# Kernel tuning notes

Hardware: AMD Instinct MI355X
Metric: run time of the kernel (lower is better)

Reference implementation:

```python
import jax, jax.numpy as jnp
import numpy as np

B = 4096
NUM_PTS = 1000

def de_boor(knotss, t, CP, p):
    # knotss: [N, K], t: [T, N], CP: [N, ncp, 2, 1] -> [T, N, 2, 1]
    N = knotss.shape[0]
    # k[b] = number of knots in knotss[b, p+1:] strictly below t (matches torch loop)
    k = jnp.sum((t[:, :, None] > knotss[None, :, p + 1:]).astype(jnp.int32), axis=-1)  # [T, N]
    bn = jnp.arange(N)[None, :, None]
    idx = k[:, :, None] + jnp.arange(p + 1)[None, None, :]           # [T, N, p+1]
    E = CP[bn, idx]                                                  # [T, N, p+1, 2, 1]
    te = t[:, :, None, None, None]
    for j in range(1, p + 1):
        m = p - j + 1
        i = jnp.arange(m)[None, None, :]
        a1 = knotss[bn, p + 1 + i + k[:, :, None]][..., None, None]  # [T, N, m, 1, 1]
        a2 = knotss[bn, i + j + k[:, :, None]][..., None, None]
        # in torch, ascending i reads old E[i+1]; vectorized update over old E is identical
        E = ((a1 - te) * E[:, :, :m] + (te - a2) * E[:, :, 1:m + 1]) / (a1 - a2)
    return E[:, :, 0]

def first_derivative(Pc, knots):
    n = Pc.shape[1]
    den = (knots[:, 4:n + 3] - knots[:, 1:n])[:, :, None, None]
    Q = 3.0 / den * (Pc[:, 1:] - Pc[:, :-1])
    return Q, knots[:, 1:-1]

def second_derivative(Q, knots):
    n = Q.shape[1]
    den = (knots[:, 3:n + 2] - knots[:, 1:n])[:, :, None, None]
    R = 2.0 / den * (Q[:, 1:] - Q[:, :-1])
    return R, knots[:, 1:-1]

def construct(t, knots, p=3):
    # t: [B], knots: [B, K] -> N: [B, K-1]; replicates stale-tail behavior of torch loop
    K = knots.shape[1]
    N = ((t[:, None] >= knots[:, :-1]) & (t[:, None] < knots[:, 1:])).astype(knots.dtype)
    lenN = K - 2
    for power in range(1, p + 1):
        m = lenN - power
        den_a = knots[:, power:power + m] - knots[:, :m]
        a = jnp.where(den_a != 0, (t[:, None] - knots[:, :m]) / jnp.where(den_a != 0, den_a, 1.0), 0.0)
        den_b = knots[:, power + 1:power + 1 + m] - knots[:, 1:1 + m]
        b = jnp.where(den_b != 0, (knots[:, power + 1:power + 1 + m] - t[:, None]) / jnp.where(den_b != 0, den_b, 1.0), 0.0)
        N = N.at[:, :m].set(N[:, :m] * a + N[:, 1:m + 1] * b)
    return N

def construct_A(knots):
    # knots: [B, 12], 6 data points -> A: [B, 8, 8]
    Bn = knots.shape[0]
    rows = [construct(knots[:, i + 3], knots) for i in range(5)]
    # i == 5 hits the knots[0, 8] == 1 branch (clamped right end): one-hot at column 7
    row5 = jnp.zeros((Bn, knots.shape[1] - 1), knots.dtype).at[:, 7].set(1.0)
    A = jnp.stack(rows + [row5], axis=1)[:, :, :8]                   # [B, 6, 8]
    z = jnp.zeros((Bn, 1, 8), knots.dtype)
    A = jnp.concatenate([z, A, z], axis=1)                           # [B, 8, 8]
    A = A.at[:, 0, 0].add(knots[:, 5]).at[:, 0, 1].add(-knots[:, 4] - knots[:, 5]).at[:, 0, 2].add(knots[:, 4])
    A = A.at[:, -1, -3].add(1.0 - knots[:, 7]).at[:, -1, -2].add(knots[:, 7] + knots[:, 6] - 2.0).at[:, -1, -1].add(1.0 - knots[:, 6])
    return A

def solve(P, knots):
    Bn = P.shape[0]
    z = jnp.zeros((Bn, 1, 1), P.dtype)
    Px = jnp.concatenate([z, P[:, :, 0], z], axis=1)  # [B, 8, 1]
    Py = jnp.concatenate([z, P[:, :, 1], z], axis=1)
    inv = jnp.linalg.inv(construct_A(knots))
    Cx = inv @ Px
    Cy = inv @ Py
    return jnp.concatenate([Cx, Cy], axis=2)[..., None]  # [B, 8, 2, 1]

def forward(x, P, W1, b1, W2, b2, W3, b3):
    h = jax.nn.relu(x @ W1.T + b1)
    h = jax.nn.relu(h @ W2.T + b2)
    xs = jax.nn.softmax(h @ W3.T + b3, axis=1)  # [B, 5]
    # torch: w[:, i] = x[:, i] + detach(w[:, i-1]) -> cumsum in value, identity in grad
    x4 = xs[:, :4]
    w = x4 + jax.lax.stop_gradient(jnp.cumsum(x4, axis=1) - x4)
    Bn = x.shape[0]
    knots = jnp.concatenate([jnp.zeros((Bn, 4), x.dtype), w, jnp.ones((Bn, 4), x.dtype)], axis=1)  # [B, 12]
    C = solve(P, knots)  # [B, 8, 2, 1]
    # global curvature over linspace(knots[0,3]=0, knots[0,10]=1, NUM_PTS)
    L = jnp.linspace(0.0, 1.0, NUM_PTS).astype(x.dtype)
    tall = jnp.broadcast_to(L[:, None], (NUM_PTS, Bn))
    Q, dk = first_derivative(C, knots)
    R, ddk = second_derivative(Q, dk)
    sp = de_boor(dk, tall, Q, 2)    # [T, B, 2, 1] spline'
    sdp = de_boor(ddk, tall, R, 1)  # [T, B, 2, 1] spline''
    spx, spy = sp[:, :, 0, 0], sp[:, :, 1, 0]
    sdx, sdy = sdp[:, :, 0, 0], sdp[:, :, 1, 0]
    speed2 = spx ** 2 + spy ** 2
    curv = (spx * sdy - spy * sdx) / (speed2 ** 3) ** 0.5
    vals = curv ** 2 * jnp.sqrt(speed2)  # [T, B]; de_boor(knots2, J, Q, 2) == spline', reused
    S1 = vals[1::2].sum(axis=0)
    S2 = vals[0::2].sum(axis=0)
    h_step = 1.0 / (NUM_PTS - 1)
    integration = h_step / 3.0 * (4.0 * S1 + 2.0 * S2)
    return integration, knots

def setup_inputs():
    key = jax.random.key(0)
    ks = jax.random.split(key, 8)
    return {
        "x": jax.random.normal(ks[0], (B, 8), jnp.float32),
        "P": jax.random.normal(ks[1], (B, 6, 2, 1), jnp.float32),
        "W1": jax.random.normal(ks[2], (128, 8), jnp.float32) * 0.3,
        "b1": jnp.full((128,), 0.01, jnp.float32),
        "W2": jax.random.normal(ks[3], (128, 128), jnp.float32) * 0.09,
        "b2": jnp.full((128,), 0.01, jnp.float32),
        "W3": jax.random.normal(ks[4], (5, 128), jnp.float32) * 0.1,
        "b3": jnp.full((5,), 0.01, jnp.float32),
    }

def reference(x, P, W1, b1, W2, b2, W3, b3):
    return forward(x, P, W1, b1, W2, b2, W3, b3)
```

## Files before the change

### kernel.cpp

```cpp
#include <hip/hip_runtime.h>
#include <math.h>

#define BATCH 4096
#define NPTS 1000

#define WSYNC() do { asm volatile("s_waitcnt lgkmcnt(0)" ::: "memory"); \
                     __builtin_amdgcn_sched_barrier(0); } while (0)

__device__ __forceinline__ float frcp(float v) { return __builtin_amdgcn_rcpf(v); }

__global__ __launch_bounds__(256, 2) void net2_one(
    const float* __restrict__ x, const float* __restrict__ P,
    const float* __restrict__ W1, const float* __restrict__ b1,
    const float* __restrict__ W2, const float* __restrict__ b2,
    const float* __restrict__ W3, const float* __restrict__ b3,
    float* __restrict__ out_integ, float* __restrict__ out_knots)
{
    __shared__ float4 s_w2[4096];
    __shared__ float s_h1[8][128];
    __shared__ float s_part[4][4][5];
    __shared__ float LA[8][8][10];
    __shared__ float LQ[8][16];
    __shared__ float LR[8][16];
    __shared__ float s_coef[8][64];

    const int tid = threadIdx.x;
    const int wv = tid >> 6, lane = tid & 63;
    const int p = tid >> 7, row = tid & 127;
    const int b0 = blockIdx.x * 8;

    {
        const float4* W2v = (const float4*)W2;
        #pragma unroll
        for (int it = 0; it < 16; ++it) {
            int f = it * 256 + tid;
            int j = f >> 5, c4 = f & 31;
            s_w2[j * 32 + (c4 ^ (j & 7))] = W2v[f];
        }
    }

    {
        float4 w0 = ((const float4*)(W1 + row * 8))[0];
        float4 w1 = ((const float4*)(W1 + row * 8))[1];
        float bb = b1[row];
        #pragma unroll
        for (int k = 0; k < 4; ++k) {
            const float* xr = x + (b0 + p * 4 + k) * 8;
            float4 xa = ((const float4*)xr)[0];
            float4 xb = ((const float4*)xr)[1];
            float h = bb + w0.x*xa.x + w0.y*xa.y + w0.z*xa.z + w0.w*xa.w
                         + w1.x*xb.x + w1.y*xb.y + w1.z*xb.z + w1.w*xb.w;
            s_h1[p * 4 + k][row] = fmaxf(h, 0.f);
        }
    }
    __syncthreads();

    float bb2 = b2[row];
    float a0 = bb2, a1 = bb2, a2 = bb2, a3 = bb2;
    {
        const float4* wrow = s_w2 + row * 32;
        const int rx = row & 7;
        const float4* h0 = (const float4*)s_h1[p * 4 + 0];
        const float4* h1 = (const float4*)s_h1[p * 4 + 1];
        const float4* h2p = (const float4*)s_h1[p * 4 + 2];
        const float4* h3 = (const float4*)s_h1[p * 4 + 3];
        #pragma unroll 8
        for (int c4 = 0; c4 < 32; ++c4) {
            float4 w = wrow[c4 ^ rx];
            float4 ha = h0[c4], hb = h1[c4], hc = h2p[c4], hd = h3[c4];
            a0 += w.x*ha.x + w.y*ha.y + w.z*ha.z + w.w*ha.w;
            a1 += w.x*hb.x + w.y*hb.y + w.z*hb.z + w.w*hb.w;
            a2 += w.x*hc.x + w.y*hc.y + w.z*hc.z + w.w*hc.w;
            a3 += w.x*hd.x + w.y*hd.y + w.z*hd.z + w.w*hd.w;
        }
    }
    float h2_0 = fmaxf(a0, 0.f), h2_1 = fmaxf(a1, 0.f);
    float h2_2 = fmaxf(a2, 0.f), h2_3 = fmaxf(a3, 0.f);

    #pragma unroll
    for (int c = 0; c < 5; ++c) {
        float wc = W3[c * 128 + row];
        float p0 = wc * h2_0, p1 = wc * h2_1, p2 = wc * h2_2, p3 = wc * h2_3;
        #pragma unroll
        for (int m = 32; m >= 1; m >>= 1) {
            p0 += __shfl_xor(p0, m, 64);
            p1 += __shfl_xor(p1, m, 64);
            p2 += __shfl_xor(p2, m, 64);
            p3 += __shfl_xor(p3, m, 64);
        }
        if (lane == 0) {
            s_part[wv][0][c] = p0; s_part[wv][1][c] = p1;
            s_part[wv][2][c] = p2; s_part[wv][3][c] = p3;
        }
    }
    __syncthreads();

    if (wv == 0) {
        const int el = lane >> 3, r = lane & 7;
        const int e = b0 + el;
        const int pw = (el >> 2) * 2;

        float lg0 = s_part[pw][el & 3][0] + s_part[pw + 1][el & 3][0] + b3[0];
        float lg1 = s_part[pw][el & 3][1] + s_part[pw + 1][el & 3][1] + b3[1];
        float lg2 = s_part[pw][el & 3][2] + s_part[pw + 1][el & 3][2] + b3[2];
        float lg3 = s_part[pw][el & 3][3] + s_part[pw + 1][el & 3][3] + b3[3];
        float lg4 = s_part[pw][el & 3][4] + s_part[pw + 1][el & 3][4] + b3[4];
        float mx = fmaxf(fmaxf(fmaxf(fmaxf(lg0, lg1), lg2), lg3), lg4);
        float e0 = expf(lg0-mx), e1 = expf(lg1-mx), e2 = expf(lg2-mx),
              e3 = expf(lg3-mx), e4 = expf(lg4-mx);
        float s = e0 + e1 + e2 + e3 + e4;
        float xs0 = e0/s, xs1 = e1/s, xs2 = e2/s, xs3 = e3/s;
        float c0 = xs0, c1 = c0 + xs1, c2 = c1 + xs2, c3 = c2 + xs3;
        float w4 = xs0 + (c0 - xs0);
        float w5 = xs1 + (c1 - xs1);
        float w6 = xs2 + (c2 - xs2);
        float w7 = xs3 + (c3 - xs3);

        {
            float kv = (r < 4) ? 0.f : (r == 4 ? w4 : r == 5 ? w5 : r == 6 ? w6 : w7);
            out_knots[e * 12 + r] = kv;
            if (r < 4) {
                out_knots[e * 12 + 8 + r] = 1.f;
                s_coef[el][60 + r] = (r == 0 ? w4 : r == 1 ? w5 : r == 2 ? w6 : w7);
            }
        }

        const float ka[12] = {0.f,0.f,0.f,0.f,w4,w5,w6,w7,1.f,1.f,1.f,1.f};
        float t = (r == 2) ? w4 : (r == 3) ? w5 : (r == 4) ? w6 : (r == 5) ? w7 : 0.f;
        float N[11];
        #pragma unroll
        for (int i = 0; i < 11; ++i)
            N[i] = (t >= ka[i] && t < ka[i+1]) ? 1.f : 0.f;
        #pragma unroll
        for (int pq = 1; pq <= 3; ++pq) {
            #pragma unroll
            for (int i = 0; i < 10; ++i) {
                if (i < 10 - pq) {
                    float da = ka[i+pq] - ka[i];
                    float av = (da != 0.f) ? (t - ka[i]) * frcp(da) : 0.f;
                    float db = ka[i+pq+1] - ka[i+1];
                    float bv = (db != 0.f) ? (ka[i+pq+1] - t) * frcp(db) : 0.f;
                    N[i] = N[i] * av + N[i+1] * bv;
                }
            }
        }

        float a[10];
        #pragma unroll
        for (int c = 0; c < 8; ++c) {
            float v0 = (c==0) ? w5 : (c==1) ? (-w4-w5) : (c==2) ? w4 : 0.f;
            float v6 = (c==7) ? 1.f : 0.f;
            float v7 = (c==5) ? (1.f-w7) : (c==6) ? (w7+w6-2.f) : (c==7) ? (1.f-w6) : 0.f;
            float vb = (r==0) ? v0 : (r==6) ? v6 : v7;
            a[c] = (r >= 1 && r <= 5) ? N[c] : vb;
        }
        {
            float px = 0.f, py = 0.f;
            if (r >= 1 && r <= 6) {
                px = P[e * 12 + (r-1) * 2 + 0];
                py = P[e * 12 + (r-1) * 2 + 1];
            }
            a[8] = px; a[9] = py;
        }

        int done = 0, pcol = 7;
        #pragma unroll
        for (int col = 0; col < 8; ++col) {
            float bv = done ? -1.f : fabsf(a[col]);
            int bi = lane;
            #pragma unroll
            for (int m = 1; m <= 4; m <<= 1) {
                float ov = __shfl_xor(bv, m, 64);
                int   oi = __shfl_xor(bi, m, 64);
                if (ov > bv || (ov == bv && oi < bi)) { bv = ov; bi = oi; }
            }
            float pr[10];
            #pragma unroll
            for (int c = 0; c < 10; ++c) pr[c] = __shfl(a[c], bi, 64);
            if (lane == bi) { done = 1; pcol = col; }
            else if (!done) {
                float f = a[col] * frcp(pr[col]);
                #pragma unroll
                for (int c = 0; c < 10; ++c) if (c > col) a[c] -= f * pr[c];
            }
        }
        #pragma unroll
        for (int c = 0; c < 10; ++c) LA[el][pcol][c] = a[c];
        WSYNC();

        if (r < 2) {
            const int par = r;
            float C[8];
            #pragma unroll
            for (int col = 7; col >= 0; --col) {
                float sv = LA[el][col][8 + par];
                #pragma unroll
                for (int c = col + 1; c < 8; ++c) sv -= LA[el][col][c] * C[c];
                C[col] = sv * frcp(LA[el][col][col]);
            }
            float Qr[7], Rr[6];
            const float dq[7] = { w4, w5, w6, w7 - w4, 1.f - w5, 1.f - w6, 1.f - w7 };
            #pragma unroll
            for (int i = 0; i < 7; ++i) Qr[i] = (3.f * frcp(dq[i])) * (C[i+1] - C[i]);
            const float dr[6] = { w4, w5, w6 - w4, w7 - w5, 1.f - w6, 1.f - w7 };
            #pragma unroll
            for (int i = 0; i < 6; ++i) Rr[i] = (2.f * frcp(dr[i])) * (Qr[i+1] - Qr[i]);
            #pragma unroll
            for (int i = 0; i < 7; ++i) LQ[el][i*2+par] = Qr[i];
            #pragma unroll
            for (int i = 0; i < 6; ++i) LR[el][i*2+par] = Rr[i];
        }
        WSYNC();

        if (r < 5) {
            const int s5 = r;
            float k2 = (s5 <= 1) ? 0.f : (s5 == 2) ? w4 : (s5 == 3) ? w5 : w6;
            float k3 = (s5 == 0) ? 0.f : (s5 == 1) ? w4 : (s5 == 2) ? w5 : (s5 == 3) ? w6 : w7;
            float k4 = (s5 == 0) ? w4 : (s5 == 1) ? w5 : (s5 == 2) ? w6 : (s5 == 3) ? w7 : 1.f;
            float k5 = (s5 == 0) ? w5 : (s5 == 1) ? w6 : (s5 == 2) ? w7 : 1.f;
            float q0x = LQ[el][s5*2],     q0y = LQ[el][s5*2+1];
            float q1x = LQ[el][(s5+1)*2], q1y = LQ[el][(s5+1)*2+1];
            float q2x = LQ[el][(s5+2)*2], q2y = LQ[el][(s5+2)*2+1];
            float r0x = LR[el][s5*2],     r0y = LR[el][s5*2+1];
            float r1x = LR[el][(s5+1)*2], r1y = LR[el][(s5+1)*2+1];
            float r42 = frcp(k4-k2), r53 = frcp(k5-k3), r43 = frcp(k4-k3);
            float A0x = (k4*q0x - k2*q1x)*r42, B0x = (q1x-q0x)*r42;
            float A1x = (k5*q1x - k3*q2x)*r53, B1x = (q2x-q1x)*r53;
            float c0x = r43*(k4*A0x - k3*A1x);
            float c1x = r43*(k4*B0x - A0x + A1x - k3*B1x);
            float c2x = r43*(B1x - B0x);
            float e0x = r43*(k4*r0x - k3*r1x);
            float e1x = r43*(r1x - r0x);
            float A0y = (k4*q0y - k2*q1y)*r42, B0y = (q1y-q0y)*r42;
            float A1y = (k5*q1y - k3*q2y)*r53, B1y = (q2y-q1y)*r53;
            float c0y = r43*(k4*A0y - k3*A1y);
            float c1y = r43*(k4*B0y - A0y + A1y - k3*B1y);
            float c2y = r43*(B1y - B0y);
            float e0y = r43*(k4*r0y - k3*r1y);
            float e1y = r43*(r1y - r0y);
            float* cb = &s_coef[el][s5 * 12];
            cb[0] = c0x; cb[1] = c1x; cb[2]  = c2x; cb[3]  = c0y;
            cb[4] = c1y; cb[5] = c2y; cb[6]  = e0x; cb[7]  = e1x;
            cb[8] = e0y; cb[9] = e1y; cb[10] = 0.f; cb[11] = 0.f;
        }
    }
    __syncthreads();

    const float c999 = 1.f / 999.f;
    #pragma unroll
    for (int q = 0; q < 2; ++q) {
        const int el = wv * 2 + q;
        const int e = b0 + el;
        float v = s_coef[el][lane];
        int vi = __float_as_int(v);
        float w4 = __int_as_float(__builtin_amdgcn_readlane(vi, 60));
        float w5 = __int_as_float(__builtin_amdgcn_readlane(vi, 61));
        float w6 = __int_as_float(__builtin_amdgcn_readlane(vi, 62));
        float w7 = __int_as_float(__builtin_amdgcn_readlane(vi, 63));

        auto bsearch = [&](float w) {
            int lo = 0, hi = 1000;
            #pragma unroll
            for (int it = 0; it < 10; ++it) {
                int mid = (lo + hi) >> 1;
                bool pr = ((float)mid * c999 > w);
                hi = pr ? mid : hi;
                lo = pr ? lo : (mid + 1);
            }
            return lo;
        };
        int B0 = bsearch(w4), B1 = bsearch(w5), B2 = bsearch(w6), B3 = bsearch(w7);

        float acc = 0.f;
        #define DOSEG(S, LOE, HIE) { \
            float cx0 = __int_as_float(__builtin_amdgcn_readlane(vi, (S)*12+0)); \
            float cx1 = __int_as_float(__builtin_amdgcn_readlane(vi, (S)*12+1)); \
            float cx2 = __int_as_float(__builtin_amdgcn_readlane(vi, (S)*12+2)); \
            float cy0 = __int_as_float(__builtin_amdgcn_readlane(vi, (S)*12+3)); \
            float cy1 = __int_as_float(__builtin_amdgcn_readlane(vi, (S)*12+4)); \
            float cy2 = __int_as_float(__builtin_amdgcn_readlane(vi, (S)*12+5)); \
            float ex0 = __int_as_float(__builtin_amdgcn_readlane(vi, (S)*12+6)); \
            float ex1 = __int_as_float(__builtin_amdgcn_readlane(vi, (S)*12+7)); \
            float ey0 = __int_as_float(__builtin_amdgcn_readlane(vi, (S)*12+8)); \
            float ey1 = __int_as_float(__builtin_amdgcn_readlane(vi, (S)*12+9)); \
            int lo = (LOE), hi = (HIE); \
            float wl = ((lo + lane) & 1) ? 4.f : 2.f; \
            for (int idx = lo + lane; idx < hi; idx += 64) { \
                float tt = (float)idx * c999; \
                float spx = (cx2 * tt + cx1) * tt + cx0; \
                float spy = (cy2 * tt + cy1) * tt + cy0; \
                float sdx = ex1 * tt + ex0; \
                float sdy = ey1 * tt + ey0; \
                float s2 = spx * spx + spy * spy; \
                float cross = spx * sdy - spy * sdx; \
                float rs = rsqrtf(s2); \
                float rs2 = rs * rs; \
                acc += wl * (cross * cross * (rs2 * rs2 * rs)); \
            } }
        DOSEG(0, 0,  B0)
        DOSEG(1, B0, B1)
        DOSEG(2, B1, B2)
        DOSEG(3, B2, B3)
        DOSEG(4, B3, 1000)
        #undef DOSEG

        #pragma unroll
        for (int m = 32; m >= 1; m >>= 1) acc += __shfl_xor(acc, m, 64);
        if (lane == 0) out_integ[e] = (1.f / 999.f) / 3.f * acc;
    }
}

extern "C" void kernel_launch(void* const* d_in, const int* in_sizes, int n_in,
                              void* d_out, int out_size, void* d_ws, size_t ws_size,
                              hipStream_t stream) {
    const float* x  = (const float*)d_in[0];
    const float* P  = (const float*)d_in[1];
    const float* W1 = (const float*)d_in[2];
    const float* b1 = (const float*)d_in[3];
    const float* W2 = (const float*)d_in[4];
    const float* b2 = (const float*)d_in[5];
    const float* W3 = (const float*)d_in[6];
    const float* b3 = (const float*)d_in[7];
    float* out_integ = (float*)d_out;
    float* out_knots = out_integ + BATCH;

    net2_one<<<dim3(BATCH / 8), dim3(256), 0, stream>>>(
        x, P, W1, b1, W2, b2, W3, b3, out_integ, out_knots);
}
```

Measured before the change: 26.29 us.

## Use 1024-thread blocks over 16 batch elements, one wave per element

Each block now has 1024 threads and handles 16 batch elements instead of 256 threads over 8. The shared W2 staging is amortized over twice as many elements, and each thread computes two MLP rows instead of four. The integration stage now gives each wave a single element instead of looping over two. There are half as many blocks, so fewer W2 loads into LDS in total, but the larger blocks and larger LDS use could reduce occupancy, and the launch bound of 1024 may restrict registers.

```diff
diff --git a/kernel.cpp b/kernel.cpp
--- a/kernel.cpp
+++ b/kernel.cpp
@@ -9,7 +9,7 @@
 
 __device__ __forceinline__ float frcp(float v) { return __builtin_amdgcn_rcpf(v); }
 
-__global__ __launch_bounds__(256, 2) void net2_one(
+__global__ __launch_bounds__(1024, 4) void net2_one(
     const float* __restrict__ x, const float* __restrict__ P,
     const float* __restrict__ W1, const float* __restrict__ b1,
     const float* __restrict__ W2, const float* __restrict__ b2,
@@ -17,23 +17,23 @@
     float* __restrict__ out_integ, float* __restrict__ out_knots)
 {
     __shared__ float4 s_w2[4096];
-    __shared__ float s_h1[8][128];
-    __shared__ float s_part[4][4][5];
-    __shared__ float LA[8][8][10];
-    __shared__ float LQ[8][16];
-    __shared__ float LR[8][16];
-    __shared__ float s_coef[8][64];
+    __shared__ float s_h1[16][128];
+    __shared__ float s_part[16][2][5];
+    __shared__ float LA[16][8][10];
+    __shared__ float LQ[16][16];
+    __shared__ float LR[16][16];
+    __shared__ float s_coef[16][64];
 
     const int tid = threadIdx.x;
     const int wv = tid >> 6, lane = tid & 63;
     const int p = tid >> 7, row = tid & 127;
-    const int b0 = blockIdx.x * 8;
+    const int b0 = blockIdx.x * 16;
 
     {
         const float4* W2v = (const float4*)W2;
         #pragma unroll
-        for (int it = 0; it < 16; ++it) {
-            int f = it * 256 + tid;
+        for (int it = 0; it < 4; ++it) {
+            int f = it * 1024 + tid;
             int j = f >> 5, c4 = f & 31;
             s_w2[j * 32 + (c4 ^ (j & 7))] = W2v[f];
         }
@@ -44,67 +44,57 @@
         float4 w1 = ((const float4*)(W1 + row * 8))[1];
         float bb = b1[row];
         #pragma unroll
-        for (int k = 0; k < 4; ++k) {
-            const float* xr = x + (b0 + p * 4 + k) * 8;
+        for (int k = 0; k < 2; ++k) {
+            const float* xr = x + (b0 + p * 2 + k) * 8;
             float4 xa = ((const float4*)xr)[0];
             float4 xb = ((const float4*)xr)[1];
             float h = bb + w0.x*xa.x + w0.y*xa.y + w0.z*xa.z + w0.w*xa.w
                          + w1.x*xb.x + w1.y*xb.y + w1.z*xb.z + w1.w*xb.w;
-            s_h1[p * 4 + k][row] = fmaxf(h, 0.f);
+            s_h1[p * 2 + k][row] = fmaxf(h, 0.f);
         }
     }
     __syncthreads();
 
     float bb2 = b2[row];
-    float a0 = bb2, a1 = bb2, a2 = bb2, a3 = bb2;
+    float a0 = bb2, a1 = bb2;
     {
         const float4* wrow = s_w2 + row * 32;
         const int rx = row & 7;
-        const float4* h0 = (const float4*)s_h1[p * 4 + 0];
-        const float4* h1 = (const float4*)s_h1[p * 4 + 1];
-        const float4* h2p = (const float4*)s_h1[p * 4 + 2];
-        const float4* h3 = (const float4*)s_h1[p * 4 + 3];
+        const float4* h0 = (const float4*)s_h1[p * 2 + 0];
+        const float4* h1 = (const float4*)s_h1[p * 2 + 1];
         #pragma unroll 8
         for (int c4 = 0; c4 < 32; ++c4) {
             float4 w = wrow[c4 ^ rx];
-            float4 ha = h0[c4], hb = h1[c4], hc = h2p[c4], hd = h3[c4];
+            float4 ha = h0[c4], hb = h1[c4];
             a0 += w.x*ha.x + w.y*ha.y + w.z*ha.z + w.w*ha.w;
             a1 += w.x*hb.x + w.y*hb.y + w.z*hb.z + w.w*hb.w;
-            a2 += w.x*hc.x + w.y*hc.y + w.z*hc.z + w.w*hc.w;
-            a3 += w.x*hd.x + w.y*hd.y + w.z*hd.z + w.w*hd.w;
         }
     }
     float h2_0 = fmaxf(a0, 0.f), h2_1 = fmaxf(a1, 0.f);
-    float h2_2 = fmaxf(a2, 0.f), h2_3 = fmaxf(a3, 0.f);
 
     #pragma unroll
     for (int c = 0; c < 5; ++c) {
         float wc = W3[c * 128 + row];
-        float p0 = wc * h2_0, p1 = wc * h2_1, p2 = wc * h2_2, p3 = wc * h2_3;
+        float p0 = wc * h2_0, p1 = wc * h2_1;
         #pragma unroll
         for (int m = 32; m >= 1; m >>= 1) {
             p0 += __shfl_xor(p0, m, 64);
             p1 += __shfl_xor(p1, m, 64);
-            p2 += __shfl_xor(p2, m, 64);
-            p3 += __shfl_xor(p3, m, 64);
-        }
-        if (lane == 0) {
-            s_part[wv][0][c] = p0; s_part[wv][1][c] = p1;
-            s_part[wv][2][c] = p2; s_part[wv][3][c] = p3;
-        }
+        }
+        if (lane == 0) { s_part[wv][0][c] = p0; s_part[wv][1][c] = p1; }
     }
     __syncthreads();
 
-    if (wv == 0) {
-        const int el = lane >> 3, r = lane & 7;
+    if (wv < 2) {
+        const int el = wv * 8 + (lane >> 3), r = lane & 7;
         const int e = b0 + el;
-        const int pw = (el >> 2) * 2;
-
-        float lg0 = s_part[pw][el & 3][0] + s_part[pw + 1][el & 3][0] + b3[0];
-        float lg1 = s_part[pw][el & 3][1] + s_part[pw + 1][el & 3][1] + b3[1];
-        float lg2 = s_part[pw][el & 3][2] + s_part[pw + 1][el & 3][2] + b3[2];
-        float lg3 = s_part[pw][el & 3][3] + s_part[pw + 1][el & 3][3] + b3[3];
-        float lg4 = s_part[pw][el & 3][4] + s_part[pw + 1][el & 3][4] + b3[4];
+        const int g2 = (el >> 1) * 2, sl = el & 1;
+
+        float lg0 = s_part[g2][sl][0] + s_part[g2 + 1][sl][0] + b3[0];
+        float lg1 = s_part[g2][sl][1] + s_part[g2 + 1][sl][1] + b3[1];
+        float lg2 = s_part[g2][sl][2] + s_part[g2 + 1][sl][2] + b3[2];
+        float lg3 = s_part[g2][sl][3] + s_part[g2 + 1][sl][3] + b3[3];
+        float lg4 = s_part[g2][sl][4] + s_part[g2 + 1][sl][4] + b3[4];
         float mx = fmaxf(fmaxf(fmaxf(fmaxf(lg0, lg1), lg2), lg3), lg4);
         float e0 = expf(lg0-mx), e1 = expf(lg1-mx), e2 = expf(lg2-mx),
               e3 = expf(lg3-mx), e4 = expf(lg4-mx);
@@ -246,12 +236,10 @@
     }
     __syncthreads();
 
-    const float c999 = 1.f / 999.f;
-    #pragma unroll
-    for (int q = 0; q < 2; ++q) {
-        const int el = wv * 2 + q;
-        const int e = b0 + el;
-        float v = s_coef[el][lane];
+    {
+        const int e = b0 + wv;
+        const float c999 = 1.f / 999.f;
+        float v = s_coef[wv][lane];
         int vi = __float_as_int(v);
         float w4 = __int_as_float(__builtin_amdgcn_readlane(vi, 60));
         float w5 = __int_as_float(__builtin_amdgcn_readlane(vi, 61));
@@ -324,6 +312,6 @@
     float* out_integ = (float*)d_out;
     float* out_knots = out_integ + BATCH;
 
-    net2_one<<<dim3(BATCH / 8), dim3(256), 0, stream>>>(
+    net2_one<<<dim3(BATCH / 16), dim3(1024), 0, stream>>>(
         x, P, W1, b1, W2, b2, W3, b3, out_integ, out_knots);
 }
```

After: 25.03 us. 1.05x faster.
